# Performance work log

Measured on AMD Instinct MI355X. Metric: run time of the kernel, lower is better.

The kernel has to match this reference:

```python
import jax, jax.numpy as jnp
import numpy as np
import math

NUM_HEADS = 16
D_MODEL = 1024
LN_EPS = 1e-5


def _layer_norm(x, g, b):
    mu = jnp.mean(x, axis=-1, keepdims=True)
    var = jnp.mean((x - mu) ** 2, axis=-1, keepdims=True)
    return (x - mu) / jnp.sqrt(var + LN_EPS) * g + b


def setup_inputs() -> dict:
    key = jax.random.key(0)
    ks = jax.random.split(key, 12)
    B, H, W, d = 32, 16, 16, D_MODEL
    P, F = 64, 128
    s = 0.02
    return {
        "x": jax.random.normal(ks[0], (B, H, W, d), jnp.float32),
        "pattern_features": jax.random.normal(ks[1], (B, P, F), jnp.float32),
        "wq": jax.random.normal(ks[2], (d, d), jnp.float32) * s,
        "bq": jnp.zeros((d,), jnp.float32),
        "wk": jax.random.normal(ks[3], (d, d), jnp.float32) * s,
        "bk": jnp.zeros((d,), jnp.float32),
        "wv": jax.random.normal(ks[4], (d, d), jnp.float32) * s,
        "bv": jnp.zeros((d,), jnp.float32),
        "wo": jax.random.normal(ks[5], (d, d), jnp.float32) * s,
        "bo": jnp.zeros((d,), jnp.float32),
        "ln_g": jnp.ones((d,), jnp.float32),
        "ln_b": jnp.zeros((d,), jnp.float32),
    }


def reference(x, pattern_features, wq, bq, wk, bk, wv, bv, wo, bo, ln_g, ln_b):
    B, H, W, d = x.shape
    S = H * W
    nh = NUM_HEADS
    dk = d // nh
    x_seq = x.reshape(B, S, d)

    def proj(w, b):
        return (x_seq @ w.T + b).reshape(B, S, nh, dk).transpose(0, 2, 1, 3)  # (B,nh,S,dk)

    q, k, v = proj(wq, bq), proj(wk, bk), proj(wv, bv)
    scores = jnp.einsum("bhsd,bhtd->bhst", q, k) / math.sqrt(dk)  # (B,nh,S,S)

    # creative bias: diversity bonus on top-left min(S,64) block, same for all heads
    m = min(S, 64)
    sim = jnp.einsum("bpf,bqf->bpq", pattern_features, pattern_features)
    div = 1.0 - jax.nn.softmax(sim, axis=-1)  # (B,P,P)
    bias = jnp.zeros((B, nh, S, S), x.dtype)
    bias = bias.at[:, :, :m, :m].set(div[:, None, :m, :m] * 0.1)

    # faithful to torch: scores + bias.unsqueeze(0) -> rank-5 (1,B,nh,S,S)
    scores5 = scores[None] + bias[None]
    aw = jax.nn.softmax(scores5, axis=-1)
    attn = jnp.matmul(aw, v)  # (1,B,nh,S,dk) via broadcasting
    # faithful to torch transpose(1,2).view(B,S,d): row-major reshape of (1,nh,B,S,dk)
    attn = jnp.transpose(attn, (0, 2, 1, 3, 4)).reshape(B, S, d)

    out = attn @ wo.T + bo
    out = _layer_norm(out + x_seq, ln_g, ln_b)

    attention_weights = jax.nn.softmax(scores, axis=-1).mean(axis=1)  # (B,S,S)
    return out.reshape(B, H, W, d), attention_weights
```

## Files before the change

kernel.cpp:

```cpp
#include <hip/hip_runtime.h>

typedef unsigned short u16;
typedef unsigned int   u32;
typedef short bf16x8 __attribute__((ext_vector_type(8)));
typedef float f32x4  __attribute__((ext_vector_type(4)));

__device__ __forceinline__ float bf2f(u16 u){
  union { u32 u; float f; } c; c.u = ((u32)u) << 16; return c.f;
}
__device__ __forceinline__ u16 f2bf(float f){
  union { float f; u32 u; } c; c.f = f;
  u32 u = c.u + 0x7fffu + ((c.u >> 16) & 1u);
  return (u16)(u >> 16);
}

__device__ __forceinline__ void gload16(const u16* g, u16* l){
  __builtin_amdgcn_global_load_lds((const __attribute__((address_space(1))) u32*)g,
                                   (__attribute__((address_space(3))) u32*)l, 16, 0, 0);
}

__device__ __forceinline__ float waveRed(float v, int ismax){
  #pragma unroll
  for (int o = 32; o > 0; o >>= 1){
    float t = __shfl_xor(v, o, 64);
    v = ismax ? fmaxf(v, t) : (v + t);
  }
  return v;
}
__device__ __forceinline__ float blockRed(float v, int ismax, float* red, int tid){
  v = waveRed(v, ismax);
  __syncthreads();
  if ((tid & 63) == 0) red[tid >> 6] = v;
  __syncthreads();
  return ismax ? fmaxf(fmaxf(red[0], red[1]), fmaxf(red[2], red[3]))
               : (red[0] + red[1] + red[2] + red[3]);
}

__global__ __launch_bounds__(256)
void conv_all(const float* __restrict__ x, const float* __restrict__ w0,
              const float* __restrict__ w1, const float* __restrict__ w2,
              const float* __restrict__ w3, u16* __restrict__ xdst,
              u16* __restrict__ wdst){
  const int bid = blockIdx.x;
  const float* s;
  u16* d;
  size_t i;
  if (bid < 4096){
    s = x; d = xdst;
    i = ((size_t)bid * 256 + threadIdx.x) * 8;
  } else {
    const int wb = bid - 4096;
    const int wi = wb >> 9;
    s = wi == 0 ? w0 : (wi == 1 ? w1 : (wi == 2 ? w2 : w3));
    d = wdst + (size_t)wi * 1048576;
    i = ((size_t)(wb & 511) * 256 + threadIdx.x) * 8;
  }
  const float4 a = *(const float4*)(s + i);
  const float4 b = *(const float4*)(s + i + 4);
  uint4 o;
  o.x = (u32)f2bf(a.x) | ((u32)f2bf(a.y) << 16);
  o.y = (u32)f2bf(a.z) | ((u32)f2bf(a.w) << 16);
  o.z = (u32)f2bf(b.x) | ((u32)f2bf(b.y) << 16);
  o.w = (u32)f2bf(b.z) | ((u32)f2bf(b.w) << 16);
  *(uint4*)(d + i) = o;
}

__global__ __launch_bounds__(256)
void div_kernel(const float* __restrict__ pf, float* __restrict__ divp)
{
  __shared__ float pfs[64][129];
  __shared__ float svs[64][65];
  const int b = blockIdx.x;
  const int tid = threadIdx.x;
  const float* pb = pf + (size_t)b * 8192;
  for (int i = tid; i < 8192; i += 256) pfs[i >> 7][i & 127] = pb[i];
  __syncthreads();
  const int p = tid & 63, qg = tid >> 6;
  for (int qq = qg * 16; qq < qg * 16 + 16; ++qq){
    float a = 0.f;
    #pragma unroll 8
    for (int f = 0; f < 128; ++f) a += pfs[p][f] * pfs[qq][f];
    svs[p][qq] = a;
  }
  __syncthreads();
  if (tid < 64){
    float m = -1e30f;
    for (int qq = 0; qq < 64; ++qq) m = fmaxf(m, svs[tid][qq]);
    float s = 0.f;
    for (int qq = 0; qq < 64; ++qq){ const float e = __expf(svs[tid][qq] - m); svs[tid][qq] = e; s += e; }
    const float inv = 1.f / s;
    float* dr = divp + ((size_t)b * 64 + tid) * 64;
    for (int qq = 0; qq < 64; ++qq) dr[qq] = 0.1f * (1.f - svs[tid][qq] * inv);
  }
}

template<int MODE>
__global__ __launch_bounds__(256, 3)
void gemm_lds(const u16* __restrict__ A, const u16* __restrict__ Wb,
              const float* __restrict__ bias0, const float* __restrict__ bias1,
              const float* __restrict__ bias2, void* __restrict__ outp)
{
  __shared__ u16 As[3][4096];
  __shared__ u16 Bs[3][4096];
  const int tid = threadIdx.x, lane = tid & 63, w = tid >> 6;
  const int wm = (w >> 1) * 64, wn = (w & 1) * 64;
  const int bmraw = blockIdx.x;
  const int bm = (bmraw & 7) * 8 + (bmraw >> 3);
  int bn = blockIdx.y;
  const u16* Wp = Wb;
  const float* bias = bias0;
  float scale = 1.f;
  int wsel = 0;
  if (MODE == 0){
    wsel = bn >> 3; bn &= 7;
    Wp = Wb + (size_t)wsel * 1048576;
    bias = wsel == 0 ? bias0 : (wsel == 1 ? bias1 : bias2);
    if (wsel == 0) scale = 0.125f;
  }
  const bool vsw = (MODE == 0 && wsel == 2);
  const int mt  = vsw ? bn : bm;
  const int nt2 = vsw ? bm : bn;
  const u16* MA = vsw ? Wp : A;
  const u16* MB = vsw ? A  : Wp;

  const f32x4 z = {0.f, 0.f, 0.f, 0.f};
  f32x4 acc[4][4];
  #pragma unroll
  for (int i = 0; i < 4; ++i)
    #pragma unroll
    for (int j = 0; j < 4; ++j) acc[i][j] = z;

  const int r4  = lane >> 2;
  const int c8s = (((lane & 3) ^ ((lane >> 3) & 3)) * 8);
  const int ca0 = w * 2, ca1 = w * 2 + 1;
  const u16* gA0 = MA + (size_t)(mt  * 128 + ca0 * 16 + r4) * 1024 + c8s;
  const u16* gA1 = MA + (size_t)(mt  * 128 + ca1 * 16 + r4) * 1024 + c8s;
  const u16* gB0 = MB + (size_t)(nt2 * 128 + ca0 * 16 + r4) * 1024 + c8s;
  const u16* gB1 = MB + (size_t)(nt2 * 128 + ca1 * 16 + r4) * 1024 + c8s;
  const int lo0 = ca0 * 512 + lane * 8;
  const int lo1 = ca1 * 512 + lane * 8;

  const int fr = lane & 15, quad = lane >> 4;
  int offA[4], offB[4];
  #pragma unroll
  for (int i = 0; i < 4; ++i){
    const int r = wm + i * 16 + fr;
    offA[i] = r * 32 + ((quad ^ ((r >> 1) & 3)) * 8);
  }
  #pragma unroll
  for (int j = 0; j < 4; ++j){
    const int r = wn + j * 16 + fr;
    offB[j] = r * 32 + ((quad ^ ((r >> 1) & 3)) * 8);
  }

#define STG(s, kk) \
    gload16(gA0 + (kk), &As[s][lo0]); \
    gload16(gA1 + (kk), &As[s][lo1]); \
    gload16(gB0 + (kk), &Bs[s][lo0]); \
    gload16(gB1 + (kk), &Bs[s][lo1]);

  STG(0, 0)
  STG(1, 32)
  asm volatile("s_waitcnt vmcnt(4)" ::: "memory");
  __builtin_amdgcn_sched_barrier(0);
  __builtin_amdgcn_s_barrier();
  asm volatile("" ::: "memory");
  __builtin_amdgcn_sched_barrier(0);

  int slot = 0;
  #pragma unroll 1
  for (int t = 0; t < 32; ++t){
    const int s2 = slot < 1 ? 2 : slot - 1;
    if (t < 30){ STG(s2, (t + 2) * 32) }
    const u16* as_ = As[slot];
    const u16* bs_ = Bs[slot];
    bf16x8 af[4], bfv[4];
    #pragma unroll
    for (int i = 0; i < 4; ++i) af[i]  = *(const bf16x8*)&as_[offA[i]];
    #pragma unroll
    for (int j = 0; j < 4; ++j) bfv[j] = *(const bf16x8*)&bs_[offB[j]];
    __builtin_amdgcn_s_setprio(1);
    #pragma unroll
    for (int i = 0; i < 4; ++i)
      #pragma unroll
      for (int j = 0; j < 4; ++j)
        acc[i][j] = __builtin_amdgcn_mfma_f32_16x16x32_bf16(af[i], bfv[j], acc[i][j], 0, 0, 0);
    __builtin_amdgcn_s_setprio(0);
    if (t < 30)       { asm volatile("s_waitcnt vmcnt(4)" ::: "memory"); }
    else if (t == 30) { asm volatile("s_waitcnt vmcnt(0)" ::: "memory"); }
    if (t < 31){
      __builtin_amdgcn_sched_barrier(0);
      __builtin_amdgcn_s_barrier();
      asm volatile("" ::: "memory");
      __builtin_amdgcn_sched_barrier(0);
    }
    slot = slot == 2 ? 0 : slot + 1;
  }
#undef STG

  #pragma unroll
  for (int i = 0; i < 4; ++i){
    #pragma unroll
    for (int j = 0; j < 4; ++j){
      const int gr0 = mt  * 128 + wm + i * 16 + quad * 4;
      const int gc  = nt2 * 128 + wn + j * 16 + fr;
      if (vsw){
        const int bb = gc >> 8, s = gc & 255;
        #pragma unroll
        for (int r = 0; r < 4; ++r){
          const int grow = gr0 + r;
          const int h = grow >> 6, kk = grow & 63;
          ((u16*)outp)[(size_t)2 * 8388608 + (size_t)bb * 262144 +
                       (size_t)h * 16384 + (size_t)kk * 256 + s] =
            f2bf(acc[i][j][r] + bias[grow]);
        }
      } else {
        const float bvv = bias[gc];
        #pragma unroll
        for (int r = 0; r < 4; ++r){
          const int gr = gr0 + r;
          const float val = (acc[i][j][r] + bvv) * scale;
          if (MODE == 0){
            const int b = gr >> 8, s = gr & 255, h = gc >> 6, kk = gc & 63;
            ((u16*)outp)[(size_t)wsel * 8388608 + (size_t)b * 262144 +
                         (size_t)h * 16384 + (size_t)s * 64 + kk] = f2bf(val);
          } else {
            ((float*)outp)[(size_t)gr * 1024 + gc] = val;
          }
        }
      }
    }
  }
}

__global__ __launch_bounds__(256, 2)
void attn_aw(const u16* __restrict__ q, const u16* __restrict__ k,
             const u16* __restrict__ vT, const float* __restrict__ divp,
             u16* __restrict__ attn_s, float* __restrict__ aw)
{
  __shared__ __align__(16) u16 Ps[4][16][136];
  const int raw = blockIdx.x;
  const int blk = (raw & 7) * 64 + (raw >> 3);
  const int b = blk >> 4, st = blk & 15;
  const int tid = threadIdx.x, lane = tid & 63, w = tid >> 6;
  const int quad = lane >> 4, l15 = lane & 15;
  const int rowb = st * 16;
  const f32x4 z = {0.f, 0.f, 0.f, 0.f};
  float awacc[16][4] = {};

  #pragma unroll 1
  for (int hi = 0; hi < 4; ++hi){
    const int h = hi * 4 + w;
    const u16* qh = q  + ((size_t)b * 16 + h) * 16384;
    const u16* kh = k  + ((size_t)b * 16 + h) * 16384;
    const u16* vh = vT + ((size_t)b * 16 + h) * 16384;
    const bf16x8 af0 = *(const bf16x8*)(qh + (size_t)(rowb + l15) * 64 + quad * 8);
    const bf16x8 af1 = *(const bf16x8*)(qh + (size_t)(rowb + l15) * 64 + 32 + quad * 8);
    f32x4 sc[16];
    #pragma unroll
    for (int ct = 0; ct < 16; ++ct){
      const bf16x8 b0 = *(const bf16x8*)(kh + (size_t)(ct * 16 + l15) * 64 + quad * 8);
      const bf16x8 b1 = *(const bf16x8*)(kh + (size_t)(ct * 16 + l15) * 64 + 32 + quad * 8);
      f32x4 a = __builtin_amdgcn_mfma_f32_16x16x32_bf16(af0, b0, z, 0, 0, 0);
      sc[ct]  = __builtin_amdgcn_mfma_f32_16x16x32_bf16(af1, b1, a, 0, 0, 0);
    }
    float rs[4];
    if (st < 4){
      #pragma unroll
      for (int rr = 0; rr < 4; ++rr){
        float m = sc[0][rr];
        #pragma unroll
        for (int ct = 1; ct < 16; ++ct) m = fmaxf(m, sc[ct][rr]);
        #pragma unroll
        for (int o = 1; o < 16; o <<= 1) m = fmaxf(m, __shfl_xor(m, o, 64));
        float s = 0.f;
        #pragma unroll
        for (int ct = 0; ct < 16; ++ct) s += __expf(sc[ct][rr] - m);
        #pragma unroll
        for (int o = 1; o < 16; o <<= 1) s += __shfl_xor(s, o, 64);
        const float inv = 1.f / s;
        #pragma unroll
        for (int ct = 0; ct < 16; ++ct)
          awacc[ct][rr] += __expf(sc[ct][rr] - m) * inv;
      }
      const float* dv = divp + (size_t)b * 4096 + (size_t)(rowb + quad * 4) * 64 + l15;
      #pragma unroll
      for (int ct = 0; ct < 4; ++ct)
        #pragma unroll
        for (int rr = 0; rr < 4; ++rr)
          sc[ct][rr] += dv[rr * 64 + ct * 16];
      #pragma unroll
      for (int rr = 0; rr < 4; ++rr){
        float m = sc[0][rr];
        #pragma unroll
        for (int ct = 1; ct < 16; ++ct) m = fmaxf(m, sc[ct][rr]);
        #pragma unroll
        for (int o = 1; o < 16; o <<= 1) m = fmaxf(m, __shfl_xor(m, o, 64));
        float s = 0.f;
        #pragma unroll
        for (int ct = 0; ct < 16; ++ct){
          const float e = __expf(sc[ct][rr] - m); sc[ct][rr] = e; s += e;
        }
        #pragma unroll
        for (int o = 1; o < 16; o <<= 1) s += __shfl_xor(s, o, 64);
        rs[rr] = 1.f / s;
      }
    } else {
      #pragma unroll
      for (int rr = 0; rr < 4; ++rr){
        float m = sc[0][rr];
        #pragma unroll
        for (int ct = 1; ct < 16; ++ct) m = fmaxf(m, sc[ct][rr]);
        #pragma unroll
        for (int o = 1; o < 16; o <<= 1) m = fmaxf(m, __shfl_xor(m, o, 64));
        float s = 0.f;
        #pragma unroll
        for (int ct = 0; ct < 16; ++ct){
          const float e = __expf(sc[ct][rr] - m); sc[ct][rr] = e; s += e;
        }
        #pragma unroll
        for (int o = 1; o < 16; o <<= 1) s += __shfl_xor(s, o, 64);
        rs[rr] = 1.f / s;
        #pragma unroll
        for (int ct = 0; ct < 16; ++ct)
          awacc[ct][rr] += sc[ct][rr] * rs[rr];
      }
    }
    f32x4 o4[4] = {z, z, z, z};
    #pragma unroll
    for (int half = 0; half < 2; ++half){
      #pragma unroll
      for (int ct = 0; ct < 8; ++ct)
        #pragma unroll
        for (int rr = 0; rr < 4; ++rr)
          Ps[w][quad * 4 + rr][ct * 16 + l15] = f2bf(sc[half * 8 + ct][rr] * rs[rr]);
      #pragma unroll
      for (int kc = 0; kc < 4; ++kc){
        const bf16x8 pa = *(const bf16x8*)&Ps[w][l15][kc * 32 + quad * 8];
        #pragma unroll
        for (int nt = 0; nt < 4; ++nt){
          const bf16x8 vb8 = *(const bf16x8*)(vh + (size_t)(nt * 16 + l15) * 256 +
                                              half * 128 + kc * 32 + quad * 8);
          o4[nt] = __builtin_amdgcn_mfma_f32_16x16x32_bf16(pa, vb8, o4[nt], 0, 0, 0);
        }
      }
    }
    const size_t rbase = ((size_t)(512 * h + 16 * b + st)) * 1024;
    #pragma unroll
    for (int nt = 0; nt < 4; ++nt)
      #pragma unroll
      for (int rr = 0; rr < 4; ++rr)
        attn_s[rbase + (size_t)(quad * 4 + rr) * 64 + nt * 16 + l15] = f2bf(o4[nt][rr]);
  }

  float* awl = (float*)&Ps[0][0][0];
  const size_t base = (size_t)b * 65536 + (size_t)rowb * 256;
  #pragma unroll
  for (int cc = 0; cc < 4; ++cc){
    __syncthreads();
    #pragma unroll
    for (int j = 0; j < 4; ++j)
      #pragma unroll
      for (int rr = 0; rr < 4; ++rr)
        awl[(w * 16 + quad * 4 + rr) * 68 + j * 16 + l15] = awacc[cc * 4 + j][rr];
    __syncthreads();
    const int idx = tid * 4;
    const int row = idx >> 6, col = idx & 63;
    const float4 a0 = *(const float4*)&awl[(      row) * 68 + col];
    const float4 a1 = *(const float4*)&awl[(16  + row) * 68 + col];
    const float4 a2 = *(const float4*)&awl[(32  + row) * 68 + col];
    const float4 a3 = *(const float4*)&awl[(48  + row) * 68 + col];
    float4 o;
    o.x = (a0.x + a1.x + a2.x + a3.x) * 0.0625f;
    o.y = (a0.y + a1.y + a2.y + a3.y) * 0.0625f;
    o.z = (a0.z + a1.z + a2.z + a3.z) * 0.0625f;
    o.w = (a0.w + a1.w + a2.w + a3.w) * 0.0625f;
    *(float4*)(aw + base + (size_t)row * 256 + cc * 64 + col) = o;
  }
}

__global__ __launch_bounds__(256)
void ln_kernel(const float* __restrict__ y2, const float* __restrict__ x,
               const float* __restrict__ g, const float* __restrict__ bb,
               float* __restrict__ outp)
{
  __shared__ float red[4];
  const int r = blockIdx.x, tid = threadIdx.x;
  const float4 yv = ((const float4*)(y2 + (size_t)r * 1024))[tid];
  const float4 xv = ((const float4*)(x  + (size_t)r * 1024))[tid];
  const float v0 = yv.x + xv.x;
  const float v1 = yv.y + xv.y;
  const float v2 = yv.z + xv.z;
  const float v3 = yv.w + xv.w;
  const float ssum = blockRed(v0 + v1 + v2 + v3, 0, red, tid);
  const float mu = ssum * (1.f / 1024.f);
  const float d0 = v0 - mu, d1 = v1 - mu, d2 = v2 - mu, d3 = v3 - mu;
  const float sq = blockRed(d0 * d0 + d1 * d1 + d2 * d2 + d3 * d3, 0, red, tid);
  const float rstd = rsqrtf(sq * (1.f / 1024.f) + 1e-5f);
  const float4 gv = ((const float4*)g)[tid];
  const float4 bv = ((const float4*)bb)[tid];
  float4 o;
  o.x = d0 * rstd * gv.x + bv.x;
  o.y = d1 * rstd * gv.y + bv.y;
  o.z = d2 * rstd * gv.z + bv.z;
  o.w = d3 * rstd * gv.w + bv.w;
  ((float4*)(outp + (size_t)r * 1024))[tid] = o;
}

extern "C" void kernel_launch(void* const* d_in, const int* in_sizes, int n_in,
                              void* d_out, int out_size, void* d_ws, size_t ws_size,
                              hipStream_t stream)
{
  int ix = -1, ipf = -1, iw[4] = {-1,-1,-1,-1}, iv[6] = {-1,-1,-1,-1,-1,-1};
  int nw = 0, nv = 0;
  for (int i = 0; i < n_in; ++i){
    const int sz = in_sizes[i];
    if (sz == 8388608 && ix < 0) ix = i;
    else if (sz == 262144 && ipf < 0) ipf = i;
    else if (sz == 1048576 && nw < 4) iw[nw++] = i;
    else if (sz == 1024 && nv < 6) iv[nv++] = i;
  }
  if (ix < 0 || ipf < 0 || nw != 4 || nv != 6){
    ix = 0; ipf = 1; iw[0] = 2; iv[0] = 3; iw[1] = 4; iv[1] = 5;
    iw[2] = 6; iv[2] = 7; iw[3] = 8; iv[3] = 9; iv[4] = 10; iv[5] = 11;
  }

  const float* x   = (const float*)d_in[ix];
  const float* pf  = (const float*)d_in[ipf];
  const float* wq  = (const float*)d_in[iw[0]];
  const float* wk  = (const float*)d_in[iw[1]];
  const float* wv  = (const float*)d_in[iw[2]];
  const float* wo  = (const float*)d_in[iw[3]];
  const float* bq  = (const float*)d_in[iv[0]];
  const float* bk  = (const float*)d_in[iv[1]];
  const float* bv  = (const float*)d_in[iv[2]];
  const float* bo  = (const float*)d_in[iv[3]];
  const float* lng = (const float*)d_in[iv[4]];
  const float* lnb = (const float*)d_in[iv[5]];

  float* out0   = (float*)d_out;
  float* aw_out = out0 + 8388608;

  u16* x_bf = (u16*)d_out;
  u16* attn = x_bf + 8388608;
  u16* qkv    = (u16*)d_ws;
  float* divp = (float*)((char*)d_ws + (size_t)48 * 1048576);
  u16* warena = (u16*)((char*)d_ws + (size_t)49 * 1048576);
  float* y2   = (float*)d_ws;

  conv_all<<<6144, 256, 0, stream>>>(x, wq, wk, wv, wo, x_bf, warena);
  div_kernel<<<32, 256, 0, stream>>>(pf, divp);

  gemm_lds<0><<<dim3(64, 24), 256, 0, stream>>>(x_bf, warena, bq, bk, bv, (void*)qkv);

  u16* qw = qkv, *kw = qkv + 8388608, *vw = qkv + 16777216;
  attn_aw<<<512, 256, 0, stream>>>(qw, kw, vw, divp, attn, aw_out);

  gemm_lds<1><<<dim3(64, 8), 256, 0, stream>>>(attn, warena + 3145728, bo, nullptr, nullptr, (void*)y2);
  ln_kernel<<<8192, 256, 0, stream>>>(y2, x, lng, lnb, out0);
}
```

Before: 321.8 us.

## Fuse biased and unbiased softmax via exp-bias scaling and LDS-accumulate attention mean

Drops the max-subtraction passes. Each score tile is exponentiated once as soon as its MFMA finishes, and unnormalized bf16 probabilities go into a full-width LDS tile. The diversity bias becomes a multiply by a precomputed exp(div), and the unbiased weights are recovered by multiplying by exp(-div). The head-averaged weights are accumulated in a shared LDS buffer instead of a 64-register array, and the PV output is normalized afterward. The aim is to cut duplicated exp/reduction work and register pressure so occupancy can rise to 3 blocks, at the cost of extra block-wide syncs, bf16-rounded attention weights and overflow risk without max subtraction.

```diff
diff --git a/kernel.cpp b/kernel.cpp
--- a/kernel.cpp
+++ b/kernel.cpp
@@ -233,12 +233,14 @@
   }
 }
 
-__global__ __launch_bounds__(256, 2)
+__global__ __launch_bounds__(256, 3)
 void attn_aw(const u16* __restrict__ q, const u16* __restrict__ k,
              const u16* __restrict__ vT, const float* __restrict__ divp,
              u16* __restrict__ attn_s, float* __restrict__ aw)
 {
-  __shared__ __align__(16) u16 Ps[4][16][136];
+  __shared__ __align__(16) u16 Ps[4][16][264];
+  __shared__ __align__(16) float awlds[16][264];
+  __shared__ float rsush[4][16];
   const int raw = blockIdx.x;
   const int blk = (raw & 7) * 64 + (raw >> 3);
   const int b = blk >> 4, st = blk & 15;
@@ -246,7 +248,24 @@
   const int quad = lane >> 4, l15 = lane & 15;
   const int rowb = st * 16;
   const f32x4 z = {0.f, 0.f, 0.f, 0.f};
-  float awacc[16][4] = {};
+
+  for (int i = tid; i < 16 * 264; i += 256) (&awlds[0][0])[i] = 0.f;
+
+  float edvv[4][4];
+  float iedv[16];
+  if (st < 4){
+    const float* dv = divp + (size_t)b * 4096 + (size_t)(rowb + quad * 4) * 64 + l15;
+    #pragma unroll
+    for (int ct = 0; ct < 4; ++ct)
+      #pragma unroll
+      for (int rr = 0; rr < 4; ++rr)
+        edvv[ct][rr] = __expf(dv[rr * 64 + ct * 16]);
+    if (w == 0){
+      #pragma unroll
+      for (int row = 0; row < 16; ++row)
+        iedv[row] = __expf(-divp[(size_t)b * 4096 + (size_t)(rowb + row) * 64 + lane]);
+    }
+  }
 
   #pragma unroll 1
   for (int hi = 0; hi < 4; ++hi){
@@ -256,126 +275,85 @@
     const u16* vh = vT + ((size_t)b * 16 + h) * 16384;
     const bf16x8 af0 = *(const bf16x8*)(qh + (size_t)(rowb + l15) * 64 + quad * 8);
     const bf16x8 af1 = *(const bf16x8*)(qh + (size_t)(rowb + l15) * 64 + 32 + quad * 8);
-    f32x4 sc[16];
+    float sb[4] = {0.f, 0.f, 0.f, 0.f};
+    float su[4] = {0.f, 0.f, 0.f, 0.f};
     #pragma unroll
     for (int ct = 0; ct < 16; ++ct){
       const bf16x8 b0 = *(const bf16x8*)(kh + (size_t)(ct * 16 + l15) * 64 + quad * 8);
       const bf16x8 b1 = *(const bf16x8*)(kh + (size_t)(ct * 16 + l15) * 64 + 32 + quad * 8);
-      f32x4 a = __builtin_amdgcn_mfma_f32_16x16x32_bf16(af0, b0, z, 0, 0, 0);
-      sc[ct]  = __builtin_amdgcn_mfma_f32_16x16x32_bf16(af1, b1, a, 0, 0, 0);
-    }
-    float rs[4];
-    if (st < 4){
+      f32x4 a  = __builtin_amdgcn_mfma_f32_16x16x32_bf16(af0, b0, z, 0, 0, 0);
+      f32x4 sc = __builtin_amdgcn_mfma_f32_16x16x32_bf16(af1, b1, a, 0, 0, 0);
       #pragma unroll
       for (int rr = 0; rr < 4; ++rr){
-        float m = sc[0][rr];
+        float e = __expf(sc[rr]);
+        if (st < 4){
+          su[rr] += e;
+          if (ct < 4) e *= edvv[ct][rr];
+        }
+        sb[rr] += e;
+        Ps[w][quad * 4 + rr][ct * 16 + l15] = f2bf(e);
+      }
+    }
+    #pragma unroll
+    for (int o = 1; o < 16; o <<= 1)
+      #pragma unroll
+      for (int rr = 0; rr < 4; ++rr){
+        sb[rr] += __shfl_xor(sb[rr], o, 64);
+        if (st < 4) su[rr] += __shfl_xor(su[rr], o, 64);
+      }
+    float rsb[4];
+    #pragma unroll
+    for (int rr = 0; rr < 4; ++rr){
+      rsb[rr] = 1.f / sb[rr];
+      const float rsu = (st < 4) ? (1.f / su[rr]) : rsb[rr];
+      if (l15 == 0) rsush[w][quad * 4 + rr] = rsu;
+    }
+    __syncthreads();
+
+    f32x4 o4[4] = {z, z, z, z};
+    #pragma unroll
+    for (int kc = 0; kc < 8; ++kc){
+      const bf16x8 pa = *(const bf16x8*)&Ps[w][l15][kc * 32 + quad * 8];
+      #pragma unroll
+      for (int nt = 0; nt < 4; ++nt){
+        const bf16x8 vb8 = *(const bf16x8*)(vh + (size_t)(nt * 16 + l15) * 256 +
+                                            kc * 32 + quad * 8);
+        o4[nt] = __builtin_amdgcn_mfma_f32_16x16x32_bf16(pa, vb8, o4[nt], 0, 0, 0);
+      }
+    }
+
+    {
+      const int col = w * 64 + lane;
+      #pragma unroll
+      for (int wp = 0; wp < 4; ++wp)
         #pragma unroll
-        for (int ct = 1; ct < 16; ++ct) m = fmaxf(m, sc[ct][rr]);
-        #pragma unroll
-        for (int o = 1; o < 16; o <<= 1) m = fmaxf(m, __shfl_xor(m, o, 64));
-        float s = 0.f;
-        #pragma unroll
-        for (int ct = 0; ct < 16; ++ct) s += __expf(sc[ct][rr] - m);
-        #pragma unroll
-        for (int o = 1; o < 16; o <<= 1) s += __shfl_xor(s, o, 64);
-        const float inv = 1.f / s;
-        #pragma unroll
-        for (int ct = 0; ct < 16; ++ct)
-          awacc[ct][rr] += __expf(sc[ct][rr] - m) * inv;
-      }
-      const float* dv = divp + (size_t)b * 4096 + (size_t)(rowb + quad * 4) * 64 + l15;
-      #pragma unroll
-      for (int ct = 0; ct < 4; ++ct)
-        #pragma unroll
-        for (int rr = 0; rr < 4; ++rr)
-          sc[ct][rr] += dv[rr * 64 + ct * 16];
-      #pragma unroll
-      for (int rr = 0; rr < 4; ++rr){
-        float m = sc[0][rr];
-        #pragma unroll
-        for (int ct = 1; ct < 16; ++ct) m = fmaxf(m, sc[ct][rr]);
-        #pragma unroll
-        for (int o = 1; o < 16; o <<= 1) m = fmaxf(m, __shfl_xor(m, o, 64));
-        float s = 0.f;
-        #pragma unroll
-        for (int ct = 0; ct < 16; ++ct){
-          const float e = __expf(sc[ct][rr] - m); sc[ct][rr] = e; s += e;
+        for (int row = 0; row < 16; ++row){
+          float p = bf2f(Ps[wp][row][col]) * rsush[wp][row];
+          if (st < 4 && w == 0) p *= iedv[row];
+          awlds[row][col] += p;
         }
-        #pragma unroll
-        for (int o = 1; o < 16; o <<= 1) s += __shfl_xor(s, o, 64);
-        rs[rr] = 1.f / s;
-      }
-    } else {
-      #pragma unroll
-      for (int rr = 0; rr < 4; ++rr){
-        float m = sc[0][rr];
-        #pragma unroll
-        for (int ct = 1; ct < 16; ++ct) m = fmaxf(m, sc[ct][rr]);
-        #pragma unroll
-        for (int o = 1; o < 16; o <<= 1) m = fmaxf(m, __shfl_xor(m, o, 64));
-        float s = 0.f;
-        #pragma unroll
-        for (int ct = 0; ct < 16; ++ct){
-          const float e = __expf(sc[ct][rr] - m); sc[ct][rr] = e; s += e;
-        }
-        #pragma unroll
-        for (int o = 1; o < 16; o <<= 1) s += __shfl_xor(s, o, 64);
-        rs[rr] = 1.f / s;
-        #pragma unroll
-        for (int ct = 0; ct < 16; ++ct)
-          awacc[ct][rr] += sc[ct][rr] * rs[rr];
-      }
-    }
-    f32x4 o4[4] = {z, z, z, z};
-    #pragma unroll
-    for (int half = 0; half < 2; ++half){
-      #pragma unroll
-      for (int ct = 0; ct < 8; ++ct)
-        #pragma unroll
-        for (int rr = 0; rr < 4; ++rr)
-          Ps[w][quad * 4 + rr][ct * 16 + l15] = f2bf(sc[half * 8 + ct][rr] * rs[rr]);
-      #pragma unroll
-      for (int kc = 0; kc < 4; ++kc){
-        const bf16x8 pa = *(const bf16x8*)&Ps[w][l15][kc * 32 + quad * 8];
-        #pragma unroll
-        for (int nt = 0; nt < 4; ++nt){
-          const bf16x8 vb8 = *(const bf16x8*)(vh + (size_t)(nt * 16 + l15) * 256 +
-                                              half * 128 + kc * 32 + quad * 8);
-          o4[nt] = __builtin_amdgcn_mfma_f32_16x16x32_bf16(pa, vb8, o4[nt], 0, 0, 0);
-        }
-      }
-    }
+    }
+    __syncthreads();
+
     const size_t rbase = ((size_t)(512 * h + 16 * b + st)) * 1024;
     #pragma unroll
     for (int nt = 0; nt < 4; ++nt)
       #pragma unroll
       for (int rr = 0; rr < 4; ++rr)
-        attn_s[rbase + (size_t)(quad * 4 + rr) * 64 + nt * 16 + l15] = f2bf(o4[nt][rr]);
-  }
-
-  float* awl = (float*)&Ps[0][0][0];
+        attn_s[rbase + (size_t)(quad * 4 + rr) * 64 + nt * 16 + l15] =
+          f2bf(o4[nt][rr] * rsb[rr]);
+  }
+
   const size_t base = (size_t)b * 65536 + (size_t)rowb * 256;
   #pragma unroll
   for (int cc = 0; cc < 4; ++cc){
-    __syncthreads();
-    #pragma unroll
-    for (int j = 0; j < 4; ++j)
-      #pragma unroll
-      for (int rr = 0; rr < 4; ++rr)
-        awl[(w * 16 + quad * 4 + rr) * 68 + j * 16 + l15] = awacc[cc * 4 + j][rr];
-    __syncthreads();
-    const int idx = tid * 4;
-    const int row = idx >> 6, col = idx & 63;
-    const float4 a0 = *(const float4*)&awl[(      row) * 68 + col];
-    const float4 a1 = *(const float4*)&awl[(16  + row) * 68 + col];
-    const float4 a2 = *(const float4*)&awl[(32  + row) * 68 + col];
-    const float4 a3 = *(const float4*)&awl[(48  + row) * 68 + col];
+    const int idx = cc * 1024 + tid * 4;
+    const int row = idx >> 8, col = idx & 255;
+    const float4 v = *(const float4*)&awlds[row][col];
     float4 o;
-    o.x = (a0.x + a1.x + a2.x + a3.x) * 0.0625f;
-    o.y = (a0.y + a1.y + a2.y + a3.y) * 0.0625f;
-    o.z = (a0.z + a1.z + a2.z + a3.z) * 0.0625f;
-    o.w = (a0.w + a1.w + a2.w + a3.w) * 0.0625f;
-    *(float4*)(aw + base + (size_t)row * 256 + cc * 64 + col) = o;
+    o.x = v.x * 0.0625f; o.y = v.y * 0.0625f;
+    o.z = v.z * 0.0625f; o.w = v.w * 0.0625f;
+    *(float4*)(aw + base + (size_t)row * 256 + col) = o;
   }
 }
 
```

Result: faster. 309.8 us (-3.7%).
